# Optimization experiments

Measured on AMD Instinct MI355X. Metric: run time of the kernel, lower is better.

Reference implementation:

```python
import jax, jax.numpy as jnp
import numpy as np


def _reflect_pad_1(x):
    # reflect by 1 on last dim: [x1, x0..xn-1, xn-2] (size>=2 assumed)
    return jnp.concatenate([x[..., 1:2], x, x[..., -2:-1]], axis=-1)


def _lwt53_fwd_lastdim(x):
    even = x[..., 0::2]
    odd = x[..., 1::2]
    ee = _reflect_pad_1(even)
    pred = 0.5 * (ee[..., :-2] + ee[..., 2:])
    d = odd - pred
    de = _reflect_pad_1(d)
    upd = 0.25 * (de[..., :-2] + de[..., 2:])
    s = even + upd
    return s, d


def _lwt53_fwd_axis(x, axis):
    if axis in (-1, x.ndim - 1):
        return _lwt53_fwd_lastdim(x)
    xp = jnp.swapaxes(x, axis, -1)
    s, d = _lwt53_fwd_lastdim(xp)
    return jnp.swapaxes(s, axis, -1), jnp.swapaxes(d, axis, -1)


def setup_inputs() -> dict:
    key = jax.random.key(0)
    x = jax.random.normal(key, (8, 32, 512, 512), dtype=jnp.float32)
    return {"x": x}


def reference(x):
    # H, W even -> no padding branch. x: [B, C, H, W]
    s_row, d_row = _lwt53_fwd_axis(x, 3)       # each [B, C, H, W//2]
    LL, LH = _lwt53_fwd_axis(s_row, 2)          # [B, C, H//2, W//2]
    HL, HH = _lwt53_fwd_axis(d_row, 2)
    return jnp.concatenate([LL, LH, HL, HH], axis=1)  # [B, 4C, H//2, W//2]
```

## Files before the change

### kernel.cpp

```cpp
#include <hip/hip_runtime.h>

#define H   512
#define W   512
#define HP  256
#define WP  256
#define JSEG 32
#define SEGS (HP / JSEG)
#define IMGS 256

__device__ __forceinline__ float dr_scalar(const float* __restrict__ p, int k) {
    int a  = (k == 0)   ? 2   : (2 * k - 2);
    int b2 = (k == 255) ? 508 : (2 * k + 2);
    return p[2 * k + 1] - 0.5f * (p[a] + p[b2]);
}

__device__ __forceinline__ void row_lift(const float* __restrict__ p, int c, bool mainPath,
                                         float& s, float& d) {
    if (mainPath) {
        float2 vm2 = *(const float2*)(p + 2 * c - 4);
        float2 vm1 = *(const float2*)(p + 2 * c - 2);
        float2 v0  = *(const float2*)(p + 2 * c);
        float2 vp1 = *(const float2*)(p + 2 * c + 2);
        float2 vp2 = *(const float2*)(p + 2 * c + 4);
        float dm = vm1.y - 0.5f * (vm2.x + v0.x);
        float d0 = v0.y  - 0.5f * (vm1.x + vp1.x);
        float dp = vp1.y - 0.5f * (v0.x  + vp2.x);
        s = v0.x + 0.25f * (dm + dp);
        d = d0;
    } else {
        int cm = (c == 0)   ? 1   : c - 1;
        int cp = (c == 255) ? 254 : c + 1;
        float dm = dr_scalar(p, cm);
        float d0 = dr_scalar(p, c);
        float dp = dr_scalar(p, cp);
        s = p[2 * c] + 0.25f * (dm + dp);
        d = d0;
    }
}

__global__ __launch_bounds__(256, 8)
void lwt53_2d_fused(const float* __restrict__ x, float* __restrict__ out) {
    const int c   = threadIdx.x;
    const int img = blockIdx.x / SEGS;
    const int seg = blockIdx.x % SEGS;
    const int j0  = seg * JSEG;

    const float* ib = x + (size_t)img * (H * W);
    const int b  = img >> 5;
    const int ch = img & 31;
    float* const outLL = out + (((size_t)b * 128 +  0 + ch) << 16) + c;
    float* const outLH = out + (((size_t)b * 128 + 32 + ch) << 16) + c;
    float* const outHL = out + (((size_t)b * 128 + 64 + ch) << 16) + c;
    float* const outHH = out + (((size_t)b * 128 + 96 + ch) << 16) + c;

    float e1s = 0.f, e2s = 0.f, o1s = 0.f, dc1s = 0.f, dc2s = 0.f;
    float e1d = 0.f, e2d = 0.f, o1d = 0.f, dc1d = 0.f, dc2d = 0.f;

    const int js = (seg == 0) ? 0 : (j0 - 2);
    const int je = j0 + JSEG + 1;

    const bool mainPath = (c >= 2) && (c <= 253);
    const bool firstSeg = (seg == 0);

    for (int j = js; j <= je; ++j) {
        float es, ed, os, od;
        if (j <= HP - 1) {
            const float* p0 = ib + (size_t)(2 * j) * W;
            row_lift(p0,     c, mainPath, es, ed);
            row_lift(p0 + W, c, mainPath, os, od);
        } else {
            es = e2s; ed = e2d;
            os = 0.f; od = 0.f;
        }

        float dnew_s, dnew_d;
        if (j == 257) {
            dnew_s = dc2s; dnew_d = dc2d;
        } else {
            float e2s_eff = (firstSeg && j == 1) ? es : e2s;
            float e2d_eff = (firstSeg && j == 1) ? ed : e2d;
            dnew_s = o1s - 0.5f * (e2s_eff + es);
            dnew_d = o1d - 0.5f * (e2d_eff + ed);
        }

        const int rD = j - 1;
        if (rD >= j0 && rD < j0 + JSEG) {
            outLH[rD * WP] = dnew_s;
            outHH[rD * WP] = dnew_d;
        }

        float dc2s_eff = (firstSeg && j == 2) ? dnew_s : dc2s;
        float dc2d_eff = (firstSeg && j == 2) ? dnew_d : dc2d;
        float snew_s = e2s + 0.25f * (dc2s_eff + dnew_s);
        float snew_d = e2d + 0.25f * (dc2d_eff + dnew_d);

        const int rS = j - 2;
        if (rS >= j0 && rS < j0 + JSEG) {
            outLL[rS * WP] = snew_s;
            outHL[rS * WP] = snew_d;
        }

        dc2s = dc1s; dc1s = dnew_s; e2s = e1s; e1s = es; o1s = os;
        dc2d = dc1d; dc1d = dnew_d; e2d = e1d; e1d = ed; o1d = od;
    }
}

extern "C" void kernel_launch(void* const* d_in, const int* in_sizes, int n_in,
                              void* d_out, int out_size, void* d_ws, size_t ws_size,
                              hipStream_t stream) {
    const float* x = (const float*)d_in[0];
    float* out = (float*)d_out;
    dim3 grid(IMGS * SEGS);
    dim3 block(256);
    hipLaunchKernelGGL(lwt53_2d_fused, grid, block, 0, stream, x, out);
}
```

Baseline: 512.3 us.

## Process two output columns per thread with float4 loads and software-pipelined rows

Each thread now handles two output columns, reading three float4 values per row instead of five float2 values, and handles the boundary reflection with select flags in place of a scalar fallback path. Row loads are double-buffered so the next row pair is fetched while the current one is computed. Outputs are written as float2 nontemporal stores, and the segment length is halved to keep the grid size up with 128-thread blocks. This trades more halo recomputation per segment and more registers for fewer, wider memory transactions and better latency hiding.

After: 460.2 us. 1.11x faster.

```diff
diff --git a/kernel.cpp b/kernel.cpp
--- a/kernel.cpp
+++ b/kernel.cpp
@@ -1,46 +1,49 @@
 #include <hip/hip_runtime.h>
 
-#define H   512
-#define W   512
-#define HP  256
-#define WP  256
-#define JSEG 32
+#define H    512
+#define W    512
+#define HP   256
+#define WP   256
+#define JSEG 16
 #define SEGS (HP / JSEG)
 #define IMGS 256
 
-__device__ __forceinline__ float dr_scalar(const float* __restrict__ p, int k) {
-    int a  = (k == 0)   ? 2   : (2 * k - 2);
-    int b2 = (k == 255) ? 508 : (2 * k + 2);
-    return p[2 * k + 1] - 0.5f * (p[a] + p[b2]);
+typedef __attribute__((ext_vector_type(2))) float f32x2;
+
+__device__ __forceinline__ void rowlift2(float4 Lm1, float4 L0, float4 Lp1,
+                                         bool edgeL, bool edgeR,
+                                         float& s0, float& d0, float& s1, float& d1)
+{
+    float dmv = Lm1.w - 0.5f * (Lm1.x + L0.x);
+    float d0v = L0.y  - 0.5f * (Lm1.z + L0.z);
+    float d1v = L0.w  - 0.5f * (L0.x  + Lp1.x);
+    float dpv = Lp1.y - 0.5f * (L0.z  + Lp1.z);
+    if (edgeL) dmv = d1v;
+    if (edgeR) dpv = d0v;
+    s0 = L0.x + 0.25f * (dmv + d1v);
+    s1 = L0.z + 0.25f * (d0v + dpv);
+    d0 = d0v; d1 = d1v;
 }
 
-__device__ __forceinline__ void row_lift(const float* __restrict__ p, int c, bool mainPath,
-                                         float& s, float& d) {
-    if (mainPath) {
-        float2 vm2 = *(const float2*)(p + 2 * c - 4);
-        float2 vm1 = *(const float2*)(p + 2 * c - 2);
-        float2 v0  = *(const float2*)(p + 2 * c);
-        float2 vp1 = *(const float2*)(p + 2 * c + 2);
-        float2 vp2 = *(const float2*)(p + 2 * c + 4);
-        float dm = vm1.y - 0.5f * (vm2.x + v0.x);
-        float d0 = v0.y  - 0.5f * (vm1.x + vp1.x);
-        float dp = vp1.y - 0.5f * (v0.x  + vp2.x);
-        s = v0.x + 0.25f * (dm + dp);
-        d = d0;
+__device__ __forceinline__ void colstep(float e_in, float o_in,
+    float& e1, float& e2, float& o1, float& dc1, float& dc2,
+    bool firstSeg, int j, float& dnew, float& snew)
+{
+    if (j == 257) {
+        dnew = dc2;
     } else {
-        int cm = (c == 0)   ? 1   : c - 1;
-        int cp = (c == 255) ? 254 : c + 1;
-        float dm = dr_scalar(p, cm);
-        float d0 = dr_scalar(p, c);
-        float dp = dr_scalar(p, cp);
-        s = p[2 * c] + 0.25f * (dm + dp);
-        d = d0;
+        float e2e = (firstSeg && j == 1) ? e_in : e2;
+        dnew = o1 - 0.5f * (e2e + e_in);
     }
+    float dc2e = (firstSeg && j == 2) ? dnew : dc2;
+    snew = e2 + 0.25f * (dc2e + dnew);
+    dc2 = dc1; dc1 = dnew; e2 = e1; e1 = e_in; o1 = o_in;
 }
 
-__global__ __launch_bounds__(256, 8)
-void lwt53_2d_fused(const float* __restrict__ x, float* __restrict__ out) {
-    const int c   = threadIdx.x;
+__global__ __launch_bounds__(128, 4)
+void lwt53_2d_fused(const float* __restrict__ x, float* __restrict__ out)
+{
+    const int t   = threadIdx.x;
     const int img = blockIdx.x / SEGS;
     const int seg = blockIdx.x % SEGS;
     const int j0  = seg * JSEG;
@@ -48,61 +51,83 @@
     const float* ib = x + (size_t)img * (H * W);
     const int b  = img >> 5;
     const int ch = img & 31;
-    float* const outLL = out + (((size_t)b * 128 +  0 + ch) << 16) + c;
-    float* const outLH = out + (((size_t)b * 128 + 32 + ch) << 16) + c;
-    float* const outHL = out + (((size_t)b * 128 + 64 + ch) << 16) + c;
-    float* const outHH = out + (((size_t)b * 128 + 96 + ch) << 16) + c;
+    const int col = 2 * t;
+    float* const outLL = out + (((size_t)b * 128 +  0 + ch) << 16) + col;
+    float* const outLH = out + (((size_t)b * 128 + 32 + ch) << 16) + col;
+    float* const outHL = out + (((size_t)b * 128 + 64 + ch) << 16) + col;
+    float* const outHH = out + (((size_t)b * 128 + 96 + ch) << 16) + col;
 
-    float e1s = 0.f, e2s = 0.f, o1s = 0.f, dc1s = 0.f, dc2s = 0.f;
-    float e1d = 0.f, e2d = 0.f, o1d = 0.f, dc1d = 0.f, dc2d = 0.f;
+    const int om1 = 4 * (t == 0   ? 0   : t - 1);
+    const int o0  = 4 * t;
+    const int op1 = 4 * (t == 127 ? 127 : t + 1);
+    const bool edgeL = (t == 0);
+    const bool edgeR = (t == 127);
+
+    float e1s0=0,e2s0=0,o1s0=0,dc1s0=0,dc2s0=0;
+    float e1d0=0,e2d0=0,o1d0=0,dc1d0=0,dc2d0=0;
+    float e1s1=0,e2s1=0,o1s1=0,dc1s1=0,dc2s1=0;
+    float e1d1=0,e2d1=0,o1d1=0,dc1d1=0,dc2d1=0;
 
     const int js = (seg == 0) ? 0 : (j0 - 2);
     const int je = j0 + JSEG + 1;
+    const bool firstSeg = (seg == 0);
+    const int jload_max = (je < HP - 1) ? je : (HP - 1);
 
-    const bool mainPath = (c >= 2) && (c <= 253);
-    const bool firstSeg = (seg == 0);
+    float4 AE0,AE1,AE2, AO0,AO1,AO2;
+    float4 BE0,BE1,BE2, BO0,BO1,BO2;
 
-    for (int j = js; j <= je; ++j) {
-        float es, ed, os, od;
-        if (j <= HP - 1) {
-            const float* p0 = ib + (size_t)(2 * j) * W;
-            row_lift(p0,     c, mainPath, es, ed);
-            row_lift(p0 + W, c, mainPath, os, od);
-        } else {
-            es = e2s; ed = e2d;
-            os = 0.f; od = 0.f;
-        }
+#define LOADPAIR(JN, E0,E1,E2,O0,O1,O2) do {                       \
+        int jn_ = (JN);                                            \
+        if (jn_ <= jload_max) {                                    \
+            const float* rb_ = ib + (size_t)(2 * jn_) * W;         \
+            E0 = *(const float4*)(rb_ + om1);                      \
+            E1 = *(const float4*)(rb_ + o0);                       \
+            E2 = *(const float4*)(rb_ + op1);                      \
+            O0 = *(const float4*)(rb_ + W + om1);                  \
+            O1 = *(const float4*)(rb_ + W + o0);                   \
+            O2 = *(const float4*)(rb_ + W + op1);                  \
+        }                                                          \
+    } while (0)
 
-        float dnew_s, dnew_d;
-        if (j == 257) {
-            dnew_s = dc2s; dnew_d = dc2d;
-        } else {
-            float e2s_eff = (firstSeg && j == 1) ? es : e2s;
-            float e2d_eff = (firstSeg && j == 1) ? ed : e2d;
-            dnew_s = o1s - 0.5f * (e2s_eff + es);
-            dnew_d = o1d - 0.5f * (e2d_eff + ed);
-        }
+#define BODY(J, E0,E1,E2,O0,O1,O2) do {                                        \
+        const int j_ = (J);                                                    \
+        float es0,ed0,es1,ed1, os0,od0,os1,od1;                                \
+        if (j_ <= HP - 1) {                                                    \
+            rowlift2(E0,E1,E2, edgeL, edgeR, es0, ed0, es1, ed1);              \
+            rowlift2(O0,O1,O2, edgeL, edgeR, os0, od0, os1, od1);              \
+        } else {                                                               \
+            es0 = e2s0; ed0 = e2d0; es1 = e2s1; ed1 = e2d1;    \
+            os0 = od0 = os1 = od1 = 0.f;                                       \
+        }                                                                      \
+        float dns0,sns0, dnd0,snd0, dns1,sns1, dnd1,snd1;                      \
+        colstep(es0, os0, e1s0,e2s0,o1s0,dc1s0,dc2s0, firstSeg, j_, dns0, sns0); \
+        colstep(ed0, od0, e1d0,e2d0,o1d0,dc1d0,dc2d0, firstSeg, j_, dnd0, snd0); \
+        colstep(es1, os1, e1s1,e2s1,o1s1,dc1s1,dc2s1, firstSeg, j_, dns1, sns1); \
+        colstep(ed1, od1, e1d1,e2d1,o1d1,dc1d1,dc2d1, firstSeg, j_, dnd1, snd1); \
+        const int rD_ = j_ - 1;                                                \
+        if (rD_ >= j0 && rD_ < j0 + JSEG) {                                    \
+            f32x2 vLH = {dns0, dns1}; f32x2 vHH = {dnd0, dnd1};                \
+            __builtin_nontemporal_store(vLH, (f32x2*)(outLH + (size_t)rD_ * WP)); \
+            __builtin_nontemporal_store(vHH, (f32x2*)(outHH + (size_t)rD_ * WP)); \
+        }                                                                      \
+        const int rS_ = j_ - 2;                                                \
+        if (rS_ >= j0 && rS_ < j0 + JSEG) {                                    \
+            f32x2 vLL = {sns0, sns1}; f32x2 vHL = {snd0, snd1};                \
+            __builtin_nontemporal_store(vLL, (f32x2*)(outLL + (size_t)rS_ * WP)); \
+            __builtin_nontemporal_store(vHL, (f32x2*)(outHL + (size_t)rS_ * WP)); \
+        }                                                                      \
+    } while (0)
 
-        const int rD = j - 1;
-        if (rD >= j0 && rD < j0 + JSEG) {
-            outLH[rD * WP] = dnew_s;
-            outHH[rD * WP] = dnew_d;
-        }
+    LOADPAIR(js, AE0,AE1,AE2,AO0,AO1,AO2);
+    for (int j = js; j <= je; j += 2) {
+        LOADPAIR(j + 1, BE0,BE1,BE2,BO0,BO1,BO2);
+        BODY(j, AE0,AE1,AE2,AO0,AO1,AO2);
+        LOADPAIR(j + 2, AE0,AE1,AE2,AO0,AO1,AO2);
+        BODY(j + 1, BE0,BE1,BE2,BO0,BO1,BO2);
+    }
 
-        float dc2s_eff = (firstSeg && j == 2) ? dnew_s : dc2s;
-        float dc2d_eff = (firstSeg && j == 2) ? dnew_d : dc2d;
-        float snew_s = e2s + 0.25f * (dc2s_eff + dnew_s);
-        float snew_d = e2d + 0.25f * (dc2d_eff + dnew_d);
-
-        const int rS = j - 2;
-        if (rS >= j0 && rS < j0 + JSEG) {
-            outLL[rS * WP] = snew_s;
-            outHL[rS * WP] = snew_d;
-        }
-
-        dc2s = dc1s; dc1s = dnew_s; e2s = e1s; e1s = es; o1s = os;
-        dc2d = dc1d; dc1d = dnew_d; e2d = e1d; e1d = ed; o1d = od;
-    }
+#undef LOADPAIR
+#undef BODY
 }
 
 extern "C" void kernel_launch(void* const* d_in, const int* in_sizes, int n_in,
@@ -111,6 +136,6 @@
     const float* x = (const float*)d_in[0];
     float* out = (float*)d_out;
     dim3 grid(IMGS * SEGS);
-    dim3 block(256);
+    dim3 block(128);
     hipLaunchKernelGGL(lwt53_2d_fused, grid, block, 0, stream, x, out);
 }
```
